# Kernel tuning notes

Measured on AMD Instinct MI355X. Metric: run time of the kernel, lower is better.

## Reference

```python
import jax, jax.numpy as jnp
import numpy as np

N_NODES = 50000
N_EDGES = 800000
N_FEAT = 128
HIDDEN = 64
EMBED = 300
N_CLASSES = 10
N_GRAPHS = 500
LEAKY_SLOPE = 0.01  # torch F.leaky_relu default


def gcn_conv(x, W, b, src, dst, n_nodes):
    # PyG GCNConv: h = x @ W; add self-loops; norm = deg^{-1/2}[src] * deg^{-1/2}[dst]
    h = x @ W  # [N, H]
    deg = jax.ops.segment_sum(jnp.ones_like(dst, dtype=h.dtype), dst, num_segments=n_nodes) + 1.0  # +1 self-loop
    dis = jax.lax.rsqrt(deg)  # deg^{-1/2}, deg >= 1 so finite
    norm = dis[src] * dis[dst]  # [E]
    agg = jax.ops.segment_sum(h[src] * norm[:, None], dst, num_segments=n_nodes)
    agg = agg + h * (dis * dis)[:, None]  # self-loop contribution
    return agg + b


def segment_softmax(s, seg, num_segments):
    # s: [N, 1]; softmax over nodes within each graph
    m = jax.ops.segment_max(s, seg, num_segments=num_segments)
    e = jnp.exp(s - m[seg])
    z = jax.ops.segment_sum(e, seg, num_segments=num_segments)
    return e / z[seg]


def setup_inputs() -> dict:
    key = jax.random.key(0)
    ks = jax.random.split(key, 16)

    def glorot(k, shape):
        fan_in, fan_out = shape[0], shape[1]
        lim = np.sqrt(6.0 / (fan_in + fan_out)).astype(np.float32)
        return jax.random.uniform(k, shape, jnp.float32, -lim, lim)

    x = jax.random.normal(ks[0], (N_NODES, N_FEAT), jnp.float32)
    edge_index = jax.random.randint(ks[1], (2, N_EDGES), 0, N_NODES, dtype=jnp.int64)
    batch = jnp.sort(jax.random.randint(ks[2], (N_NODES,), 0, N_GRAPHS, dtype=jnp.int64))
    return {
        "x": x,
        "edge_index": edge_index,
        "batch": batch,
        "W1": glorot(ks[3], (N_FEAT, HIDDEN)),
        "b1": jnp.zeros((HIDDEN,), jnp.float32),
        "W2": glorot(ks[4], (HIDDEN, HIDDEN)),
        "b2": jnp.zeros((HIDDEN,), jnp.float32),
        "att_w": glorot(ks[5], (HIDDEN, 1)),
        "att_b": jnp.zeros((1,), jnp.float32),
        "proj_w": glorot(ks[6], (HIDDEN, EMBED)),
        "proj_b": jnp.zeros((EMBED,), jnp.float32),
        "cls_w1": glorot(ks[7], (EMBED, 128)),
        "cls_b1": jnp.zeros((128,), jnp.float32),
        "cls_w2": glorot(ks[8], (128, N_CLASSES)),
        "cls_b2": jnp.zeros((N_CLASSES,), jnp.float32),
    }


def reference(x, edge_index, batch, W1, b1, W2, b2, att_w, att_b, proj_w, proj_b, cls_w1, cls_b1, cls_w2, cls_b2):
    src, dst = edge_index[0], edge_index[1]
    n_nodes = x.shape[0]
    h = jax.nn.relu(gcn_conv(x, W1, b1, src, dst, n_nodes))
    # dropout is identity in eval mode
    h = jax.nn.relu(gcn_conv(h, W2, b2, src, dst, n_nodes))  # [N, H]
    att = jax.nn.leaky_relu(h @ att_w + att_b, negative_slope=LEAKY_SLOPE)  # [N, 1]
    att = segment_softmax(att, batch, N_GRAPHS)
    g = jax.ops.segment_sum(att * h, batch, num_segments=N_GRAPHS)  # [G, H]
    g = g @ proj_w + proj_b  # [G, EMBED]
    out = jax.nn.relu(g @ cls_w1 + cls_b1) @ cls_w2 + cls_b2  # [G, num_classes]
    return out
```

## Files before the change

### kernel.cpp

```cpp
#include <hip/hip_runtime.h>
#include <hip/hip_fp16.h>
#include <math.h>

#define N_NODES   50000
#define N_EDGES   800000
#define N_FEAT    128
#define HIDDEN    64
#define EMBED     300
#define N_CLASSES 10
#define N_GRAPHS  500
#define LEAKY     0.01f
#define SCAN_BLOCKS 196
#define NB_FILL   3125
#define NB_G2     12500

typedef __attribute__((ext_vector_type(4))) _Float16 half4f;
typedef __attribute__((ext_vector_type(8))) _Float16 half8;
typedef __attribute__((ext_vector_type(4))) float f32x4;

__device__ __forceinline__ float pk_w(unsigned p) {
    return __half2float(__ushort_as_half((unsigned short)(p >> 16)));
}

__global__ void kA(int* deg, int* gs, int* ge,
                   const float* __restrict__ W1, __half* __restrict__ W1T,
                   const float* __restrict__ W2, __half* __restrict__ W2T) {
    int bid = blockIdx.x, tid = threadIdx.x;
    if (bid < 196) {
        int i = bid * 256 + tid;
        if (i < N_NODES) deg[i] = 0;
        if (i < N_GRAPHS) { gs[i] = 0; ge[i] = 0; }
    } else if (bid < 228) {
        int idx = (bid - 196) * 256 + tid;
        int n = idx >> 7, k = idx & 127;
        W1T[idx] = __float2half(W1[k * HIDDEN + n]);
    } else {
        int idx = (bid - 228) * 256 + tid;
        int n = idx >> 6, k = idx & 63;
        W2T[idx] = __float2half(W2[k * HIDDEN + n]);
    }
}

__global__ void k_deg_rank(const int* __restrict__ dst, int* deg, int* rank) {
    int e = blockIdx.x * 256 + threadIdx.x;
    if (e < N_EDGES) rank[e] = atomicAdd(&deg[dst[e]], 1);
}

__global__ __launch_bounds__(256) void k_scan1(const int* __restrict__ deg, int* row_start,
                                               int* partials, float* dis) {
    __shared__ int wsum[4];
    int i = blockIdx.x * 256 + threadIdx.x;
    int v = (i < N_NODES) ? deg[i] : 0;
    int lane = threadIdx.x & 63, wid = threadIdx.x >> 6;
    int s = v;
    #pragma unroll
    for (int off = 1; off < 64; off <<= 1) {
        int t = __shfl_up(s, off, 64);
        if (lane >= off) s += t;
    }
    if (lane == 63) wsum[wid] = s;
    __syncthreads();
    int woff = 0;
    for (int w = 0; w < wid; ++w) woff += wsum[w];
    if (i < N_NODES) {
        row_start[i] = woff + s - v;
        dis[i] = rsqrtf((float)(deg[i] + 1));
    }
    if (threadIdx.x == 255) partials[blockIdx.x] = woff + s;
}

__global__ __launch_bounds__(256) void k_scan3b(int* row_start, const int* __restrict__ partials) {
    __shared__ int wsum[4];
    int bid = blockIdx.x, tid = threadIdx.x;
    int lane = tid & 63, wid = tid >> 6;
    int v = (tid < SCAN_BLOCKS && tid < bid) ? partials[tid] : 0;
    #pragma unroll
    for (int off = 32; off > 0; off >>= 1) v += __shfl_xor(v, off, 64);
    if (lane == 0) wsum[wid] = v;
    __syncthreads();
    int prefix = wsum[0] + wsum[1] + wsum[2] + wsum[3];
    int i = bid * 256 + tid;
    if (i < N_NODES) row_start[i] += prefix;
    if (i == 0) row_start[N_NODES] = N_EDGES;
}

__global__ __launch_bounds__(256) void kB(const int* __restrict__ src, const int* __restrict__ dst,
                                          const int* __restrict__ rank, const int* __restrict__ row_start,
                                          const float* __restrict__ dis, unsigned* __restrict__ pk,
                                          const float* __restrict__ x, const __half* __restrict__ W1T,
                                          __half* __restrict__ h1) {
    if (blockIdx.x < NB_FILL) {
        int e = blockIdx.x * 256 + threadIdx.x;
        if (e < N_EDGES) {
            int s = src[e], d = dst[e];
            float w = dis[s] * dis[d];
            unsigned short wh = __half_as_ushort(__float2half(w));
            pk[row_start[d] + rank[e]] = (unsigned)s | ((unsigned)wh << 16);
        }
        return;
    }
    int tid = threadIdx.x, wid = tid >> 6, lane = tid & 63;
    int r16 = lane & 15, kg = lane >> 4;
    int rowbase = (blockIdx.x - NB_FILL) * 64 + wid * 16;
    int arow = rowbase + r16;
    bool avalid = arow < N_NODES;
    const float* xr = x + (size_t)arow * N_FEAT;

    half8 a[4];
    #pragma unroll
    for (int kt = 0; kt < 4; ++kt) {
        int k0 = kt * 32 + kg * 8;
        float4 u = avalid ? *(const float4*)(xr + k0)     : make_float4(0.f, 0.f, 0.f, 0.f);
        float4 v = avalid ? *(const float4*)(xr + k0 + 4) : make_float4(0.f, 0.f, 0.f, 0.f);
        a[kt][0] = (_Float16)u.x; a[kt][1] = (_Float16)u.y;
        a[kt][2] = (_Float16)u.z; a[kt][3] = (_Float16)u.w;
        a[kt][4] = (_Float16)v.x; a[kt][5] = (_Float16)v.y;
        a[kt][6] = (_Float16)v.z; a[kt][7] = (_Float16)v.w;
    }
    #pragma unroll
    for (int nt = 0; nt < 4; ++nt) {
        f32x4 acc = {0.f, 0.f, 0.f, 0.f};
        const _Float16* wp = (const _Float16*)W1T + (size_t)(nt * 16 + r16) * N_FEAT + kg * 8;
        #pragma unroll
        for (int kt = 0; kt < 4; ++kt) {
            half8 b = *(const half8*)(wp + kt * 32);
            acc = __builtin_amdgcn_mfma_f32_16x16x32_f16(a[kt], b, acc, 0, 0, 0);
        }
        int col = nt * 16 + r16;
        #pragma unroll
        for (int r = 0; r < 4; ++r) {
            int row = rowbase + kg * 4 + r;
            if (row < N_NODES) h1[(size_t)row * HIDDEN + col] = __float2half(acc[r]);
        }
    }
}

__device__ __forceinline__ void gather4pk(const __half* __restrict__ h,
                                          const unsigned* __restrict__ pk,
                                          int s, int e, int lane, int g4, int q,
                                          float4& acc) {
    for (int cs = s; cs < e; cs += 64) {
        unsigned pkv = (cs + lane < e) ? pk[cs + lane] : 0u;
        int avail = e - cs; if (avail > 64) avail = 64;
        int iters = (avail + 3) >> 2;
        #pragma unroll 2
        for (int t = 0; t < iters; ++t) {
            unsigned p = __shfl(pkv, t * 4 + g4, 64);
            float w = pk_w(p);
            half4f hv = *(const half4f*)(h + ((size_t)(p & 0xFFFFu)) * HIDDEN + (q << 2));
            acc.x = fmaf(w, (float)hv.x, acc.x);
            acc.y = fmaf(w, (float)hv.y, acc.y);
            acc.z = fmaf(w, (float)hv.z, acc.z);
            acc.w = fmaf(w, (float)hv.w, acc.w);
        }
    }
}

__device__ __forceinline__ void xreduce(float4& a) {
    a.x += __shfl_xor(a.x, 16, 64); a.y += __shfl_xor(a.y, 16, 64);
    a.z += __shfl_xor(a.z, 16, 64); a.w += __shfl_xor(a.w, 16, 64);
    a.x += __shfl_xor(a.x, 32, 64); a.y += __shfl_xor(a.y, 32, 64);
    a.z += __shfl_xor(a.z, 32, 64); a.w += __shfl_xor(a.w, 32, 64);
}

__global__ __launch_bounds__(256) void k_gg(const __half* __restrict__ h1,
                                            const unsigned* __restrict__ pk,
                                            const int* __restrict__ row_start,
                                            const float* __restrict__ dis,
                                            const float* __restrict__ b1,
                                            const __half* __restrict__ W2T,
                                            __half* __restrict__ h2) {
    __shared__ __align__(16) __half sa[16 * 72];
    int tid = threadIdx.x, wid = tid >> 6, lane = tid & 63;
    int g4 = lane >> 4, q = lane & 15;
    int base = blockIdx.x * 16 + wid * 4;
    #pragma unroll
    for (int i = 0; i < 4; ++i) {
        int node = base + i;
        int s = row_start[node], e = row_start[node + 1];
        float4 acc = {0.f, 0.f, 0.f, 0.f};
        gather4pk(h1, pk, s, e, lane, g4, q, acc);
        xreduce(acc);
        float dv = dis[node], dd = dv * dv;
        half4f sv = *(const half4f*)(h1 + (size_t)node * HIDDEN + (q << 2));
        float4 bv = *(const float4*)(b1 + (q << 2));
        if (g4 == 0) {
            half4f r;
            r.x = (_Float16)fmaxf(fmaf((float)sv.x, dd, bv.x) + acc.x, 0.f);
            r.y = (_Float16)fmaxf(fmaf((float)sv.y, dd, bv.y) + acc.y, 0.f);
            r.z = (_Float16)fmaxf(fmaf((float)sv.z, dd, bv.z) + acc.z, 0.f);
            r.w = (_Float16)fmaxf(fmaf((float)sv.w, dd, bv.w) + acc.w, 0.f);
            *(half4f*)&sa[(wid * 4 + i) * 72 + (q << 2)] = r;
        }
    }
    __syncthreads();

    int r16 = lane & 15, kg = lane >> 4;
    f32x4 acc = {0.f, 0.f, 0.f, 0.f};
    const _Float16* wp = (const _Float16*)W2T + (size_t)(wid * 16 + r16) * HIDDEN + kg * 8;
    #pragma unroll
    for (int kt = 0; kt < 2; ++kt) {
        half8 a = *(const half8*)&sa[r16 * 72 + kt * 32 + kg * 8];
        half8 b = *(const half8*)(wp + kt * 32);
        acc = __builtin_amdgcn_mfma_f32_16x16x32_f16(a, b, acc, 0, 0, 0);
    }
    int col = wid * 16 + r16;
    int nodebase = blockIdx.x * 16;
    #pragma unroll
    for (int r = 0; r < 4; ++r) {
        int row = nodebase + kg * 4 + r;
        h2[(size_t)row * HIDDEN + col] = __float2half(acc[r]);
    }
}

__global__ __launch_bounds__(256) void kC(const __half* __restrict__ h2,
                                          const unsigned* __restrict__ pk,
                                          const int* __restrict__ row_start,
                                          const float* __restrict__ dis,
                                          const float* __restrict__ b2,
                                          const float* __restrict__ att_w,
                                          const float* __restrict__ att_b,
                                          __half* __restrict__ agg2,
                                          float* __restrict__ att_s,
                                          const int* __restrict__ batch,
                                          int* gs, int* ge) {
    if (blockIdx.x >= NB_G2) {
        int n = (blockIdx.x - NB_G2) * 256 + threadIdx.x;
        if (n < N_NODES) {
            int b = batch[n];
            if (n == 0 || batch[n - 1] != b) gs[b] = n;
            if (n == N_NODES - 1 || batch[n + 1] != b) ge[b] = n + 1;
        }
        return;
    }
    int tid = threadIdx.x, wid = tid >> 6, lane = tid & 63;
    int g4 = lane >> 4, q = lane & 15;
    int node = blockIdx.x * 4 + wid;
    int s = row_start[node], e = row_start[node + 1];
    float4 acc = {0.f, 0.f, 0.f, 0.f};
    gather4pk(h2, pk, s, e, lane, g4, q, acc);
    xreduce(acc);
    float dv = dis[node], dd = dv * dv;
    half4f sv = *(const half4f*)(h2 + (size_t)node * HIDDEN + (q << 2));
    float4 bv = *(const float4*)(b2 + (q << 2));
    float4 r;
    r.x = fmaxf(fmaf((float)sv.x, dd, bv.x) + acc.x, 0.f);
    r.y = fmaxf(fmaf((float)sv.y, dd, bv.y) + acc.y, 0.f);
    r.z = fmaxf(fmaf((float)sv.z, dd, bv.z) + acc.z, 0.f);
    r.w = fmaxf(fmaf((float)sv.w, dd, bv.w) + acc.w, 0.f);
    if (g4 == 0) {
        half4f rh;
        rh.x = (_Float16)r.x; rh.y = (_Float16)r.y;
        rh.z = (_Float16)r.z; rh.w = (_Float16)r.w;
        *(half4f*)(agg2 + (size_t)node * HIDDEN + (q << 2)) = rh;
    }

    float4 aw = *(const float4*)(att_w + (q << 2));
    float v = fmaf(r.x, aw.x, fmaf(r.y, aw.y, fmaf(r.z, aw.z, r.w * aw.w)));
    v += __shfl_xor(v, 1, 64); v += __shfl_xor(v, 2, 64);
    v += __shfl_xor(v, 4, 64); v += __shfl_xor(v, 8, 64);
    if (lane == 0) {
        float sc = v + att_b[0];
        att_s[node] = (sc > 0.0f) ? sc : LEAKY * sc;
    }
}

__global__ __launch_bounds__(256) void k_pool_head(const __half* __restrict__ agg2,
                                                   const float* __restrict__ att_s,
                                                   const int* __restrict__ gs,
                                                   const int* __restrict__ ge,
                                                   const float* __restrict__ proj_w,
                                                   const float* __restrict__ proj_b,
                                                   const float* __restrict__ cls_w1,
                                                   const float* __restrict__ cls_b1,
                                                   const float* __restrict__ cls_w2,
                                                   const float* __restrict__ cls_b2,
                                                   float* __restrict__ out) {
    __shared__ float red[4];
    __shared__ float red2[4 * 64];
    __shared__ float sG[HIDDEN];
    __shared__ float sT1[EMBED];
    __shared__ float sT2[128];
    int gid = blockIdx.x;
    int tid = threadIdx.x, f = tid & 63, w = tid >> 6;
    int s = gs[gid], e = ge[gid];

    float m = -INFINITY;
    for (int n = s + tid; n < e; n += 256) m = fmaxf(m, att_s[n]);
    #pragma unroll
    for (int o = 32; o > 0; o >>= 1) m = fmaxf(m, __shfl_xor(m, o, 64));
    if (f == 0) red[w] = m;
    __syncthreads();
    m = fmaxf(fmaxf(red[0], red[1]), fmaxf(red[2], red[3]));
    __syncthreads();

    float z = 0.0f;
    for (int n = s + tid; n < e; n += 256) z += expf(att_s[n] - m);
    #pragma unroll
    for (int o = 32; o > 0; o >>= 1) z += __shfl_xor(z, o, 64);
    if (f == 0) red[w] = z;
    __syncthreads();
    z = red[0] + red[1] + red[2] + red[3];
    float inv = (e > s) ? 1.0f / z : 0.0f;

    float acc = 0.0f;
    for (int n = s + w; n < e; n += 4)
        acc = fmaf(expf(att_s[n] - m) * inv,
                   __half2float(agg2[(size_t)n * HIDDEN + f]), acc);
    red2[w * 64 + f] = acc;
    __syncthreads();
    if (w == 0) sG[f] = red2[f] + red2[64 + f] + red2[128 + f] + red2[192 + f];
    __syncthreads();

    for (int c = tid; c < EMBED; c += 256) {
        float a = proj_b[c];
        #pragma unroll 8
        for (int k = 0; k < HIDDEN; ++k) a = fmaf(sG[k], proj_w[k * EMBED + c], a);
        sT1[c] = a;
    }
    __syncthreads();

    if (tid < 128) {
        float a = cls_b1[tid];
        for (int k = 0; k < EMBED; ++k) a = fmaf(sT1[k], cls_w1[k * 128 + tid], a);
        sT2[tid] = fmaxf(a, 0.f);
    }
    __syncthreads();

    if (tid < N_CLASSES) {
        float a = cls_b2[tid];
        #pragma unroll 8
        for (int k = 0; k < 128; ++k) a = fmaf(sT2[k], cls_w2[k * N_CLASSES + tid], a);
        out[gid * N_CLASSES + tid] = a;
    }
}

extern "C" void kernel_launch(void* const* d_in, const int* in_sizes, int n_in,
                              void* d_out, int out_size, void* d_ws, size_t ws_size,
                              hipStream_t stream) {
    const float* x      = (const float*)d_in[0];
    const int*   ei     = (const int*)d_in[1];
    const int*   batch  = (const int*)d_in[2];
    const float* W1     = (const float*)d_in[3];
    const float* b1     = (const float*)d_in[4];
    const float* W2     = (const float*)d_in[5];
    const float* b2     = (const float*)d_in[6];
    const float* att_w  = (const float*)d_in[7];
    const float* att_b  = (const float*)d_in[8];
    const float* proj_w = (const float*)d_in[9];
    const float* proj_b = (const float*)d_in[10];
    const float* cls_w1 = (const float*)d_in[11];
    const float* cls_b1 = (const float*)d_in[12];
    const float* cls_w2 = (const float*)d_in[13];
    const float* cls_b2 = (const float*)d_in[14];
    float* out = (float*)d_out;

    const int* e_src = ei;
    const int* e_dst = ei + N_EDGES;

    float* base = (float*)d_ws;
    size_t o = 0;
    float*    dis       = base + o;              o += 50048;
    int*      deg_i     = (int*)(base + o);      o += 50048;
    int*      row_start = (int*)(base + o);      o += 50080;
    int*      partials  = (int*)(base + o);      o += 256;
    unsigned* pk        = (unsigned*)(base + o); o += 800000;
    __half*   h1        = (__half*)(base + o);   o += 1600000;
    __half*   h2        = (__half*)(base + o);   o += 1600000;
    __half*   agg2      = (__half*)(base + o);   o += 1600000;
    int*      rank      = (int*)agg2;
    float*    att_s     = base + o;              o += 50048;
    int*      gs        = (int*)(base + o);      o += 512;
    int*      ge        = (int*)(base + o);      o += 512;
    __half*   W1T       = (__half*)(base + o);   o += 4096;
    __half*   W2T       = (__half*)(base + o);   o += 2048;

    const int NB_E  = (N_EDGES + 255) / 256;
    const int NB_GG = N_NODES / 16;

    kA<<<244, 256, 0, stream>>>(deg_i, gs, ge, W1, W1T, W2, W2T);
    k_deg_rank<<<NB_E, 256, 0, stream>>>(e_dst, deg_i, rank);
    k_scan1<<<SCAN_BLOCKS, 256, 0, stream>>>(deg_i, row_start, partials, dis);
    k_scan3b<<<SCAN_BLOCKS, 256, 0, stream>>>(row_start, partials);

    kB<<<NB_FILL + 782, 256, 0, stream>>>(e_src, e_dst, rank, row_start, dis, pk, x, W1T, h1);

    k_gg<<<NB_GG, 256, 0, stream>>>(h1, pk, row_start, dis, b1, W2T, h2);

    kC<<<NB_G2 + SCAN_BLOCKS, 256, 0, stream>>>(h2, pk, row_start, dis, b2, att_w, att_b,
                                                agg2, att_s, batch, gs, ge);

    k_pool_head<<<N_GRAPHS, 256, 0, stream>>>(agg2, att_s, gs, ge,
                                              proj_w, proj_b, cls_w1, cls_b1,
                                              cls_w2, cls_b2, out);
}
```

Measured before the change: 163.8 us.

## Fuse scan into single-pass decoupled lookback and gather two nodes per wave

Replaces the two-kernel prefix scan with one kernel in which each block publishes its total to a flagged 64-bit slot and spins on the totals of earlier blocks, removing a launch. The aggregation kernels now interleave the neighbour gathers of two destination nodes per wave, so more independent loads are in flight to hide gather latency. The layer-2 kernel processes 8 nodes per block, halving its grid. Risks are spin-wait deadlock if blocks are not co-resident, though 196 blocks should fit, and higher register pressure from the dual accumulators.

```diff
diff --git a/kernel.cpp b/kernel.cpp
--- a/kernel.cpp
+++ b/kernel.cpp
@@ -12,7 +12,7 @@
 #define LEAKY     0.01f
 #define SCAN_BLOCKS 196
 #define NB_FILL   3125
-#define NB_G2     12500
+#define NB_G2B    6250
 
 typedef __attribute__((ext_vector_type(4))) _Float16 half4f;
 typedef __attribute__((ext_vector_type(8))) _Float16 half8;
@@ -22,7 +22,7 @@
     return __half2float(__ushort_as_half((unsigned short)(p >> 16)));
 }
 
-__global__ void kA(int* deg, int* gs, int* ge,
+__global__ void kA(int* deg, int* gs, int* ge, unsigned long long* aggs,
                    const float* __restrict__ W1, __half* __restrict__ W1T,
                    const float* __restrict__ W2, __half* __restrict__ W2T) {
     int bid = blockIdx.x, tid = threadIdx.x;
@@ -30,6 +30,7 @@
         int i = bid * 256 + tid;
         if (i < N_NODES) deg[i] = 0;
         if (i < N_GRAPHS) { gs[i] = 0; ge[i] = 0; }
+        if (bid == 0 && tid < SCAN_BLOCKS) aggs[tid] = 0ULL;
     } else if (bid < 228) {
         int idx = (bid - 196) * 256 + tid;
         int n = idx >> 7, k = idx & 127;
@@ -46,12 +47,15 @@
     if (e < N_EDGES) rank[e] = atomicAdd(&deg[dst[e]], 1);
 }
 
-__global__ __launch_bounds__(256) void k_scan1(const int* __restrict__ deg, int* row_start,
-                                               int* partials, float* dis) {
+__global__ __launch_bounds__(256) void k_scan(const int* __restrict__ deg,
+                                              int* __restrict__ row_start,
+                                              unsigned long long* __restrict__ aggs,
+                                              float* __restrict__ dis) {
     __shared__ int wsum[4];
-    int i = blockIdx.x * 256 + threadIdx.x;
+    int bid = blockIdx.x, tid = threadIdx.x;
+    int i = bid * 256 + tid;
     int v = (i < N_NODES) ? deg[i] : 0;
-    int lane = threadIdx.x & 63, wid = threadIdx.x >> 6;
+    int lane = tid & 63, wid = tid >> 6;
     int s = v;
     #pragma unroll
     for (int off = 1; off < 64; off <<= 1) {
@@ -62,25 +66,28 @@
     __syncthreads();
     int woff = 0;
     for (int w = 0; w < wid; ++w) woff += wsum[w];
+    int total = wsum[0] + wsum[1] + wsum[2] + wsum[3];
+
+    if (tid == 0)
+        atomicExch(&aggs[bid], (1ULL << 32) | (unsigned long long)(unsigned)total);
+
+    int pv = 0;
+    if (tid < bid) {
+        unsigned long long g;
+        do { g = atomicAdd(&aggs[tid], 0ULL); } while (!(g >> 32));
+        pv = (int)(unsigned)(g & 0xFFFFFFFFULL);
+    }
+    #pragma unroll
+    for (int off = 32; off > 0; off >>= 1) pv += __shfl_xor(pv, off, 64);
+    __syncthreads();
+    if (lane == 0) wsum[wid] = pv;
+    __syncthreads();
+    int prefix = wsum[0] + wsum[1] + wsum[2] + wsum[3];
+
     if (i < N_NODES) {
-        row_start[i] = woff + s - v;
+        row_start[i] = woff + s - v + prefix;
         dis[i] = rsqrtf((float)(deg[i] + 1));
     }
-    if (threadIdx.x == 255) partials[blockIdx.x] = woff + s;
-}
-
-__global__ __launch_bounds__(256) void k_scan3b(int* row_start, const int* __restrict__ partials) {
-    __shared__ int wsum[4];
-    int bid = blockIdx.x, tid = threadIdx.x;
-    int lane = tid & 63, wid = tid >> 6;
-    int v = (tid < SCAN_BLOCKS && tid < bid) ? partials[tid] : 0;
-    #pragma unroll
-    for (int off = 32; off > 0; off >>= 1) v += __shfl_xor(v, off, 64);
-    if (lane == 0) wsum[wid] = v;
-    __syncthreads();
-    int prefix = wsum[0] + wsum[1] + wsum[2] + wsum[3];
-    int i = bid * 256 + tid;
-    if (i < N_NODES) row_start[i] += prefix;
     if (i == 0) row_start[N_NODES] = N_EDGES;
 }
 
@@ -156,6 +163,41 @@
     }
 }
 
+__device__ __forceinline__ void gather2(const __half* __restrict__ h,
+                                        const unsigned* __restrict__ pk,
+                                        int s0, int e0, int s1, int e1,
+                                        int lane, int g4, int q,
+                                        float4& a0, float4& a1) {
+    unsigned pv0 = (s0 + lane < e0) ? pk[s0 + lane] : 0u;
+    unsigned pv1 = (s1 + lane < e1) ? pk[s1 + lane] : 0u;
+    int n0 = e0 - s0; if (n0 > 64) n0 = 64; if (n0 < 0) n0 = 0;
+    int n1 = e1 - s1; if (n1 > 64) n1 = 64; if (n1 < 0) n1 = 0;
+    int it0 = (n0 + 3) >> 2, it1 = (n1 + 3) >> 2;
+    int itm = it0 > it1 ? it0 : it1;
+    for (int t = 0; t < itm; ++t) {
+        if (t < it0) {
+            unsigned p = __shfl(pv0, t * 4 + g4, 64);
+            float w = pk_w(p);
+            half4f hv = *(const half4f*)(h + ((size_t)(p & 0xFFFFu)) * HIDDEN + (q << 2));
+            a0.x = fmaf(w, (float)hv.x, a0.x);
+            a0.y = fmaf(w, (float)hv.y, a0.y);
+            a0.z = fmaf(w, (float)hv.z, a0.z);
+            a0.w = fmaf(w, (float)hv.w, a0.w);
+        }
+        if (t < it1) {
+            unsigned p = __shfl(pv1, t * 4 + g4, 64);
+            float w = pk_w(p);
+            half4f hv = *(const half4f*)(h + ((size_t)(p & 0xFFFFu)) * HIDDEN + (q << 2));
+            a1.x = fmaf(w, (float)hv.x, a1.x);
+            a1.y = fmaf(w, (float)hv.y, a1.y);
+            a1.z = fmaf(w, (float)hv.z, a1.z);
+            a1.w = fmaf(w, (float)hv.w, a1.w);
+        }
+    }
+    if (e0 - s0 > 64) gather4pk(h, pk, s0 + 64, e0, lane, g4, q, a0);
+    if (e1 - s1 > 64) gather4pk(h, pk, s1 + 64, e1, lane, g4, q, a1);
+}
+
 __device__ __forceinline__ void xreduce(float4& a) {
     a.x += __shfl_xor(a.x, 16, 64); a.y += __shfl_xor(a.y, 16, 64);
     a.z += __shfl_xor(a.z, 16, 64); a.w += __shfl_xor(a.w, 16, 64);
@@ -174,23 +216,32 @@
     int tid = threadIdx.x, wid = tid >> 6, lane = tid & 63;
     int g4 = lane >> 4, q = lane & 15;
     int base = blockIdx.x * 16 + wid * 4;
-    #pragma unroll
-    for (int i = 0; i < 4; ++i) {
-        int node = base + i;
-        int s = row_start[node], e = row_start[node + 1];
-        float4 acc = {0.f, 0.f, 0.f, 0.f};
-        gather4pk(h1, pk, s, e, lane, g4, q, acc);
-        xreduce(acc);
-        float dv = dis[node], dd = dv * dv;
-        half4f sv = *(const half4f*)(h1 + (size_t)node * HIDDEN + (q << 2));
-        float4 bv = *(const float4*)(b1 + (q << 2));
+    float4 bv = *(const float4*)(b1 + (q << 2));
+
+    #pragma unroll
+    for (int pr = 0; pr < 2; ++pr) {
+        int n0 = base + pr * 2, n1 = n0 + 1;
+        int s0 = row_start[n0], e0 = row_start[n0 + 1];
+        int s1 = row_start[n1], e1 = row_start[n1 + 1];
+        float4 a0 = {0.f, 0.f, 0.f, 0.f}, a1 = {0.f, 0.f, 0.f, 0.f};
+        gather2(h1, pk, s0, e0, s1, e1, lane, g4, q, a0, a1);
+        xreduce(a0); xreduce(a1);
         if (g4 == 0) {
-            half4f r;
-            r.x = (_Float16)fmaxf(fmaf((float)sv.x, dd, bv.x) + acc.x, 0.f);
-            r.y = (_Float16)fmaxf(fmaf((float)sv.y, dd, bv.y) + acc.y, 0.f);
-            r.z = (_Float16)fmaxf(fmaf((float)sv.z, dd, bv.z) + acc.z, 0.f);
-            r.w = (_Float16)fmaxf(fmaf((float)sv.w, dd, bv.w) + acc.w, 0.f);
-            *(half4f*)&sa[(wid * 4 + i) * 72 + (q << 2)] = r;
+            float d0 = dis[n0]; d0 *= d0;
+            float d1 = dis[n1]; d1 *= d1;
+            half4f sv0 = *(const half4f*)(h1 + (size_t)n0 * HIDDEN + (q << 2));
+            half4f sv1 = *(const half4f*)(h1 + (size_t)n1 * HIDDEN + (q << 2));
+            half4f r0, r1;
+            r0.x = (_Float16)fmaxf(fmaf((float)sv0.x, d0, bv.x) + a0.x, 0.f);
+            r0.y = (_Float16)fmaxf(fmaf((float)sv0.y, d0, bv.y) + a0.y, 0.f);
+            r0.z = (_Float16)fmaxf(fmaf((float)sv0.z, d0, bv.z) + a0.z, 0.f);
+            r0.w = (_Float16)fmaxf(fmaf((float)sv0.w, d0, bv.w) + a0.w, 0.f);
+            r1.x = (_Float16)fmaxf(fmaf((float)sv1.x, d1, bv.x) + a1.x, 0.f);
+            r1.y = (_Float16)fmaxf(fmaf((float)sv1.y, d1, bv.y) + a1.y, 0.f);
+            r1.z = (_Float16)fmaxf(fmaf((float)sv1.z, d1, bv.z) + a1.z, 0.f);
+            r1.w = (_Float16)fmaxf(fmaf((float)sv1.w, d1, bv.w) + a1.w, 0.f);
+            *(half4f*)&sa[(wid * 4 + pr * 2 + 0) * 72 + (q << 2)] = r0;
+            *(half4f*)&sa[(wid * 4 + pr * 2 + 1) * 72 + (q << 2)] = r1;
         }
     }
     __syncthreads();
@@ -224,8 +275,8 @@
                                           float* __restrict__ att_s,
                                           const int* __restrict__ batch,
                                           int* gs, int* ge) {
-    if (blockIdx.x >= NB_G2) {
-        int n = (blockIdx.x - NB_G2) * 256 + threadIdx.x;
+    if (blockIdx.x >= NB_G2B) {
+        int n = (blockIdx.x - NB_G2B) * 256 + threadIdx.x;
         if (n < N_NODES) {
             int b = batch[n];
             if (n == 0 || batch[n - 1] != b) gs[b] = n;
@@ -235,33 +286,47 @@
     }
     int tid = threadIdx.x, wid = tid >> 6, lane = tid & 63;
     int g4 = lane >> 4, q = lane & 15;
-    int node = blockIdx.x * 4 + wid;
-    int s = row_start[node], e = row_start[node + 1];
-    float4 acc = {0.f, 0.f, 0.f, 0.f};
-    gather4pk(h2, pk, s, e, lane, g4, q, acc);
-    xreduce(acc);
-    float dv = dis[node], dd = dv * dv;
-    half4f sv = *(const half4f*)(h2 + (size_t)node * HIDDEN + (q << 2));
+    int n0 = blockIdx.x * 8 + wid * 2, n1 = n0 + 1;
+    int s0 = row_start[n0], e0 = row_start[n0 + 1];
+    int s1 = row_start[n1], e1 = row_start[n1 + 1];
+    float4 a0 = {0.f, 0.f, 0.f, 0.f}, a1 = {0.f, 0.f, 0.f, 0.f};
+    gather2(h2, pk, s0, e0, s1, e1, lane, g4, q, a0, a1);
+    xreduce(a0); xreduce(a1);
+
     float4 bv = *(const float4*)(b2 + (q << 2));
-    float4 r;
-    r.x = fmaxf(fmaf((float)sv.x, dd, bv.x) + acc.x, 0.f);
-    r.y = fmaxf(fmaf((float)sv.y, dd, bv.y) + acc.y, 0.f);
-    r.z = fmaxf(fmaf((float)sv.z, dd, bv.z) + acc.z, 0.f);
-    r.w = fmaxf(fmaf((float)sv.w, dd, bv.w) + acc.w, 0.f);
+    float d0 = dis[n0]; d0 *= d0;
+    float d1 = dis[n1]; d1 *= d1;
+    half4f sv0 = *(const half4f*)(h2 + (size_t)n0 * HIDDEN + (q << 2));
+    half4f sv1 = *(const half4f*)(h2 + (size_t)n1 * HIDDEN + (q << 2));
+    float4 r0, r1;
+    r0.x = fmaxf(fmaf((float)sv0.x, d0, bv.x) + a0.x, 0.f);
+    r0.y = fmaxf(fmaf((float)sv0.y, d0, bv.y) + a0.y, 0.f);
+    r0.z = fmaxf(fmaf((float)sv0.z, d0, bv.z) + a0.z, 0.f);
+    r0.w = fmaxf(fmaf((float)sv0.w, d0, bv.w) + a0.w, 0.f);
+    r1.x = fmaxf(fmaf((float)sv1.x, d1, bv.x) + a1.x, 0.f);
+    r1.y = fmaxf(fmaf((float)sv1.y, d1, bv.y) + a1.y, 0.f);
+    r1.z = fmaxf(fmaf((float)sv1.z, d1, bv.z) + a1.z, 0.f);
+    r1.w = fmaxf(fmaf((float)sv1.w, d1, bv.w) + a1.w, 0.f);
     if (g4 == 0) {
-        half4f rh;
-        rh.x = (_Float16)r.x; rh.y = (_Float16)r.y;
-        rh.z = (_Float16)r.z; rh.w = (_Float16)r.w;
-        *(half4f*)(agg2 + (size_t)node * HIDDEN + (q << 2)) = rh;
+        half4f h0, h1v;
+        h0.x = (_Float16)r0.x; h0.y = (_Float16)r0.y; h0.z = (_Float16)r0.z; h0.w = (_Float16)r0.w;
+        h1v.x = (_Float16)r1.x; h1v.y = (_Float16)r1.y; h1v.z = (_Float16)r1.z; h1v.w = (_Float16)r1.w;
+        *(half4f*)(agg2 + (size_t)n0 * HIDDEN + (q << 2)) = h0;
+        *(half4f*)(agg2 + (size_t)n1 * HIDDEN + (q << 2)) = h1v;
     }
 
     float4 aw = *(const float4*)(att_w + (q << 2));
-    float v = fmaf(r.x, aw.x, fmaf(r.y, aw.y, fmaf(r.z, aw.z, r.w * aw.w)));
-    v += __shfl_xor(v, 1, 64); v += __shfl_xor(v, 2, 64);
-    v += __shfl_xor(v, 4, 64); v += __shfl_xor(v, 8, 64);
+    float v0 = fmaf(r0.x, aw.x, fmaf(r0.y, aw.y, fmaf(r0.z, aw.z, r0.w * aw.w)));
+    float v1 = fmaf(r1.x, aw.x, fmaf(r1.y, aw.y, fmaf(r1.z, aw.z, r1.w * aw.w)));
+    v0 += __shfl_xor(v0, 1, 64); v1 += __shfl_xor(v1, 1, 64);
+    v0 += __shfl_xor(v0, 2, 64); v1 += __shfl_xor(v1, 2, 64);
+    v0 += __shfl_xor(v0, 4, 64); v1 += __shfl_xor(v1, 4, 64);
+    v0 += __shfl_xor(v0, 8, 64); v1 += __shfl_xor(v1, 8, 64);
     if (lane == 0) {
-        float sc = v + att_b[0];
-        att_s[node] = (sc > 0.0f) ? sc : LEAKY * sc;
+        float sc0 = v0 + att_b[0];
+        float sc1 = v1 + att_b[0];
+        att_s[n0] = (sc0 > 0.0f) ? sc0 : LEAKY * sc0;
+        att_s[n1] = (sc1 > 0.0f) ? sc1 : LEAKY * sc1;
     }
 }
 
@@ -363,7 +428,7 @@
     float*    dis       = base + o;              o += 50048;
     int*      deg_i     = (int*)(base + o);      o += 50048;
     int*      row_start = (int*)(base + o);      o += 50080;
-    int*      partials  = (int*)(base + o);      o += 256;
+    unsigned long long* aggs = (unsigned long long*)(base + o); o += 512;
     unsigned* pk        = (unsigned*)(base + o); o += 800000;
     __half*   h1        = (__half*)(base + o);   o += 1600000;
     __half*   h2        = (__half*)(base + o);   o += 1600000;
@@ -378,17 +443,16 @@
     const int NB_E  = (N_EDGES + 255) / 256;
     const int NB_GG = N_NODES / 16;
 
-    kA<<<244, 256, 0, stream>>>(deg_i, gs, ge, W1, W1T, W2, W2T);
+    kA<<<244, 256, 0, stream>>>(deg_i, gs, ge, aggs, W1, W1T, W2, W2T);
     k_deg_rank<<<NB_E, 256, 0, stream>>>(e_dst, deg_i, rank);
-    k_scan1<<<SCAN_BLOCKS, 256, 0, stream>>>(deg_i, row_start, partials, dis);
-    k_scan3b<<<SCAN_BLOCKS, 256, 0, stream>>>(row_start, partials);
+    k_scan<<<SCAN_BLOCKS, 256, 0, stream>>>(deg_i, row_start, aggs, dis);
 
     kB<<<NB_FILL + 782, 256, 0, stream>>>(e_src, e_dst, rank, row_start, dis, pk, x, W1T, h1);
 
     k_gg<<<NB_GG, 256, 0, stream>>>(h1, pk, row_start, dis, b1, W2T, h2);
 
-    kC<<<NB_G2 + SCAN_BLOCKS, 256, 0, stream>>>(h2, pk, row_start, dis, b2, att_w, att_b,
-                                                agg2, att_s, batch, gs, ge);
+    kC<<<NB_G2B + SCAN_BLOCKS, 256, 0, stream>>>(h2, pk, row_start, dis, b2, att_w, att_b,
+                                                 agg2, att_s, batch, gs, ge);
 
     k_pool_head<<<N_GRAPHS, 256, 0, stream>>>(agg2, att_s, gs, ge,
                                               proj_w, proj_b, cls_w1, cls_b1,
```

After: 157.3 us. 4.0% less time.

## Merge scan into single-pass decoupled lookback and interleave four-node gathers

Applied to the files above, without the earlier changes.

Replaces the two-kernel prefix scan with one kernel in which each block publishes its total with a flag and spin-waits on the flags of earlier blocks, removing a launch. The neighbor gather now loads the edge lists of four nodes at once and interleaves their loads in a single loop, so more memory requests are in flight per wave. The second aggregation kernel now handles four nodes per wave with a quarter of the blocks. The spin-wait assumes earlier blocks are resident or already scheduled; with 196 blocks that holds on this GPU, but it adds a small risk and some atomic polling traffic.

```diff
diff --git a/kernel.cpp b/kernel.cpp
--- a/kernel.cpp
+++ b/kernel.cpp
@@ -12,7 +12,7 @@
 #define LEAKY     0.01f
 #define SCAN_BLOCKS 196
 #define NB_FILL   3125
-#define NB_G2     12500
+#define NB_G2Q    3125
 
 typedef __attribute__((ext_vector_type(4))) _Float16 half4f;
 typedef __attribute__((ext_vector_type(8))) _Float16 half8;
@@ -22,7 +22,7 @@
     return __half2float(__ushort_as_half((unsigned short)(p >> 16)));
 }
 
-__global__ void kA(int* deg, int* gs, int* ge,
+__global__ void kA(int* deg, int* gs, int* ge, unsigned long long* aggs,
                    const float* __restrict__ W1, __half* __restrict__ W1T,
                    const float* __restrict__ W2, __half* __restrict__ W2T) {
     int bid = blockIdx.x, tid = threadIdx.x;
@@ -30,6 +30,7 @@
         int i = bid * 256 + tid;
         if (i < N_NODES) deg[i] = 0;
         if (i < N_GRAPHS) { gs[i] = 0; ge[i] = 0; }
+        if (bid == 0 && tid < SCAN_BLOCKS) aggs[tid] = 0ULL;
     } else if (bid < 228) {
         int idx = (bid - 196) * 256 + tid;
         int n = idx >> 7, k = idx & 127;
@@ -46,12 +47,15 @@
     if (e < N_EDGES) rank[e] = atomicAdd(&deg[dst[e]], 1);
 }
 
-__global__ __launch_bounds__(256) void k_scan1(const int* __restrict__ deg, int* row_start,
-                                               int* partials, float* dis) {
+__global__ __launch_bounds__(256) void k_scan(const int* __restrict__ deg,
+                                              int* __restrict__ row_start,
+                                              unsigned long long* __restrict__ aggs,
+                                              float* __restrict__ dis) {
     __shared__ int wsum[4];
-    int i = blockIdx.x * 256 + threadIdx.x;
+    int bid = blockIdx.x, tid = threadIdx.x;
+    int i = bid * 256 + tid;
     int v = (i < N_NODES) ? deg[i] : 0;
-    int lane = threadIdx.x & 63, wid = threadIdx.x >> 6;
+    int lane = tid & 63, wid = tid >> 6;
     int s = v;
     #pragma unroll
     for (int off = 1; off < 64; off <<= 1) {
@@ -62,25 +66,28 @@
     __syncthreads();
     int woff = 0;
     for (int w = 0; w < wid; ++w) woff += wsum[w];
+    int total = wsum[0] + wsum[1] + wsum[2] + wsum[3];
+
+    if (tid == 0)
+        atomicExch(&aggs[bid], (1ULL << 32) | (unsigned long long)(unsigned)total);
+
+    int pv = 0;
+    if (tid < bid) {
+        unsigned long long g;
+        do { g = atomicAdd(&aggs[tid], 0ULL); } while (!(g >> 32));
+        pv = (int)(unsigned)(g & 0xFFFFFFFFULL);
+    }
+    #pragma unroll
+    for (int off = 32; off > 0; off >>= 1) pv += __shfl_xor(pv, off, 64);
+    __syncthreads();
+    if (lane == 0) wsum[wid] = pv;
+    __syncthreads();
+    int prefix = wsum[0] + wsum[1] + wsum[2] + wsum[3];
+
     if (i < N_NODES) {
-        row_start[i] = woff + s - v;
+        row_start[i] = woff + s - v + prefix;
         dis[i] = rsqrtf((float)(deg[i] + 1));
     }
-    if (threadIdx.x == 255) partials[blockIdx.x] = woff + s;
-}
-
-__global__ __launch_bounds__(256) void k_scan3b(int* row_start, const int* __restrict__ partials) {
-    __shared__ int wsum[4];
-    int bid = blockIdx.x, tid = threadIdx.x;
-    int lane = tid & 63, wid = tid >> 6;
-    int v = (tid < SCAN_BLOCKS && tid < bid) ? partials[tid] : 0;
-    #pragma unroll
-    for (int off = 32; off > 0; off >>= 1) v += __shfl_xor(v, off, 64);
-    if (lane == 0) wsum[wid] = v;
-    __syncthreads();
-    int prefix = wsum[0] + wsum[1] + wsum[2] + wsum[3];
-    int i = bid * 256 + tid;
-    if (i < N_NODES) row_start[i] += prefix;
     if (i == 0) row_start[N_NODES] = N_EDGES;
 }
 
@@ -135,6 +142,15 @@
     }
 }
 
+__device__ __forceinline__ void gacc(const __half* __restrict__ h, unsigned p, int q, float4& a) {
+    float w = pk_w(p);
+    half4f hv = *(const half4f*)(h + ((size_t)(p & 0xFFFFu)) * HIDDEN + (q << 2));
+    a.x = fmaf(w, (float)hv.x, a.x);
+    a.y = fmaf(w, (float)hv.y, a.y);
+    a.z = fmaf(w, (float)hv.z, a.z);
+    a.w = fmaf(w, (float)hv.w, a.w);
+}
+
 __device__ __forceinline__ void gather4pk(const __half* __restrict__ h,
                                           const unsigned* __restrict__ pk,
                                           int s, int e, int lane, int g4, int q,
@@ -144,16 +160,39 @@
         int avail = e - cs; if (avail > 64) avail = 64;
         int iters = (avail + 3) >> 2;
         #pragma unroll 2
-        for (int t = 0; t < iters; ++t) {
-            unsigned p = __shfl(pkv, t * 4 + g4, 64);
-            float w = pk_w(p);
-            half4f hv = *(const half4f*)(h + ((size_t)(p & 0xFFFFu)) * HIDDEN + (q << 2));
-            acc.x = fmaf(w, (float)hv.x, acc.x);
-            acc.y = fmaf(w, (float)hv.y, acc.y);
-            acc.z = fmaf(w, (float)hv.z, acc.z);
-            acc.w = fmaf(w, (float)hv.w, acc.w);
-        }
-    }
+        for (int t = 0; t < iters; ++t)
+            gacc(h, __shfl(pkv, t * 4 + g4, 64), q, acc);
+    }
+}
+
+__device__ __forceinline__ void gather4x(const __half* __restrict__ h,
+                                         const unsigned* __restrict__ pk,
+                                         const int rs[5], int lane, int g4, int q,
+                                         float4 a[4]) {
+    unsigned pv0 = (rs[0] + lane < rs[1]) ? pk[rs[0] + lane] : 0u;
+    unsigned pv1 = (rs[1] + lane < rs[2]) ? pk[rs[1] + lane] : 0u;
+    unsigned pv2 = (rs[2] + lane < rs[3]) ? pk[rs[2] + lane] : 0u;
+    unsigned pv3 = (rs[3] + lane < rs[4]) ? pk[rs[3] + lane] : 0u;
+    int n0 = rs[1] - rs[0]; if (n0 > 64) n0 = 64;
+    int n1 = rs[2] - rs[1]; if (n1 > 64) n1 = 64;
+    int n2 = rs[3] - rs[2]; if (n2 > 64) n2 = 64;
+    int n3 = rs[4] - rs[3]; if (n3 > 64) n3 = 64;
+    int it0 = (n0 + 3) >> 2, it1 = (n1 + 3) >> 2;
+    int it2 = (n2 + 3) >> 2, it3 = (n3 + 3) >> 2;
+    int m01 = it0 > it1 ? it0 : it1;
+    int m23 = it2 > it3 ? it2 : it3;
+    int itm = m01 > m23 ? m01 : m23;
+    for (int t = 0; t < itm; ++t) {
+        int sl = t * 4 + g4;
+        if (t < it0) gacc(h, __shfl(pv0, sl, 64), q, a[0]);
+        if (t < it1) gacc(h, __shfl(pv1, sl, 64), q, a[1]);
+        if (t < it2) gacc(h, __shfl(pv2, sl, 64), q, a[2]);
+        if (t < it3) gacc(h, __shfl(pv3, sl, 64), q, a[3]);
+    }
+    if (rs[1] - rs[0] > 64) gather4pk(h, pk, rs[0] + 64, rs[1], lane, g4, q, a[0]);
+    if (rs[2] - rs[1] > 64) gather4pk(h, pk, rs[1] + 64, rs[2], lane, g4, q, a[1]);
+    if (rs[3] - rs[2] > 64) gather4pk(h, pk, rs[2] + 64, rs[3], lane, g4, q, a[2]);
+    if (rs[4] - rs[3] > 64) gather4pk(h, pk, rs[3] + 64, rs[4], lane, g4, q, a[3]);
 }
 
 __device__ __forceinline__ void xreduce(float4& a) {
@@ -174,22 +213,29 @@
     int tid = threadIdx.x, wid = tid >> 6, lane = tid & 63;
     int g4 = lane >> 4, q = lane & 15;
     int base = blockIdx.x * 16 + wid * 4;
-    #pragma unroll
-    for (int i = 0; i < 4; ++i) {
-        int node = base + i;
-        int s = row_start[node], e = row_start[node + 1];
-        float4 acc = {0.f, 0.f, 0.f, 0.f};
-        gather4pk(h1, pk, s, e, lane, g4, q, acc);
-        xreduce(acc);
-        float dv = dis[node], dd = dv * dv;
-        half4f sv = *(const half4f*)(h1 + (size_t)node * HIDDEN + (q << 2));
-        float4 bv = *(const float4*)(b1 + (q << 2));
-        if (g4 == 0) {
+    int rs[5];
+    #pragma unroll
+    for (int i = 0; i < 5; ++i) rs[i] = row_start[base + i];
+
+    float4 a[4];
+    #pragma unroll
+    for (int i = 0; i < 4; ++i) a[i] = make_float4(0.f, 0.f, 0.f, 0.f);
+    gather4x(h1, pk, rs, lane, g4, q, a);
+    #pragma unroll
+    for (int i = 0; i < 4; ++i) xreduce(a[i]);
+
+    float4 bv = *(const float4*)(b1 + (q << 2));
+    if (g4 == 0) {
+        #pragma unroll
+        for (int i = 0; i < 4; ++i) {
+            int node = base + i;
+            float dd = dis[node]; dd *= dd;
+            half4f sv = *(const half4f*)(h1 + (size_t)node * HIDDEN + (q << 2));
             half4f r;
-            r.x = (_Float16)fmaxf(fmaf((float)sv.x, dd, bv.x) + acc.x, 0.f);
-            r.y = (_Float16)fmaxf(fmaf((float)sv.y, dd, bv.y) + acc.y, 0.f);
-            r.z = (_Float16)fmaxf(fmaf((float)sv.z, dd, bv.z) + acc.z, 0.f);
-            r.w = (_Float16)fmaxf(fmaf((float)sv.w, dd, bv.w) + acc.w, 0.f);
+            r.x = (_Float16)fmaxf(fmaf((float)sv.x, dd, bv.x) + a[i].x, 0.f);
+            r.y = (_Float16)fmaxf(fmaf((float)sv.y, dd, bv.y) + a[i].y, 0.f);
+            r.z = (_Float16)fmaxf(fmaf((float)sv.z, dd, bv.z) + a[i].z, 0.f);
+            r.w = (_Float16)fmaxf(fmaf((float)sv.w, dd, bv.w) + a[i].w, 0.f);
             *(half4f*)&sa[(wid * 4 + i) * 72 + (q << 2)] = r;
         }
     }
@@ -200,9 +246,9 @@
     const _Float16* wp = (const _Float16*)W2T + (size_t)(wid * 16 + r16) * HIDDEN + kg * 8;
     #pragma unroll
     for (int kt = 0; kt < 2; ++kt) {
-        half8 a = *(const half8*)&sa[r16 * 72 + kt * 32 + kg * 8];
+        half8 av = *(const half8*)&sa[r16 * 72 + kt * 32 + kg * 8];
         half8 b = *(const half8*)(wp + kt * 32);
-        acc = __builtin_amdgcn_mfma_f32_16x16x32_f16(a, b, acc, 0, 0, 0);
+        acc = __builtin_amdgcn_mfma_f32_16x16x32_f16(av, b, acc, 0, 0, 0);
     }
     int col = wid * 16 + r16;
     int nodebase = blockIdx.x * 16;
@@ -224,8 +270,8 @@
                                           float* __restrict__ att_s,
                                           const int* __restrict__ batch,
                                           int* gs, int* ge) {
-    if (blockIdx.x >= NB_G2) {
-        int n = (blockIdx.x - NB_G2) * 256 + threadIdx.x;
+    if (blockIdx.x >= NB_G2Q) {
+        int n = (blockIdx.x - NB_G2Q) * 256 + threadIdx.x;
         if (n < N_NODES) {
             int b = batch[n];
             if (n == 0 || batch[n - 1] != b) gs[b] = n;
@@ -235,33 +281,44 @@
     }
     int tid = threadIdx.x, wid = tid >> 6, lane = tid & 63;
     int g4 = lane >> 4, q = lane & 15;
-    int node = blockIdx.x * 4 + wid;
-    int s = row_start[node], e = row_start[node + 1];
-    float4 acc = {0.f, 0.f, 0.f, 0.f};
-    gather4pk(h2, pk, s, e, lane, g4, q, acc);
-    xreduce(acc);
-    float dv = dis[node], dd = dv * dv;
-    half4f sv = *(const half4f*)(h2 + (size_t)node * HIDDEN + (q << 2));
+    int base = blockIdx.x * 16 + wid * 4;
+    int rs[5];
+    #pragma unroll
+    for (int i = 0; i < 5; ++i) rs[i] = row_start[base + i];
+
+    float4 a[4];
+    #pragma unroll
+    for (int i = 0; i < 4; ++i) a[i] = make_float4(0.f, 0.f, 0.f, 0.f);
+    gather4x(h2, pk, rs, lane, g4, q, a);
+    #pragma unroll
+    for (int i = 0; i < 4; ++i) xreduce(a[i]);
+
     float4 bv = *(const float4*)(b2 + (q << 2));
-    float4 r;
-    r.x = fmaxf(fmaf((float)sv.x, dd, bv.x) + acc.x, 0.f);
-    r.y = fmaxf(fmaf((float)sv.y, dd, bv.y) + acc.y, 0.f);
-    r.z = fmaxf(fmaf((float)sv.z, dd, bv.z) + acc.z, 0.f);
-    r.w = fmaxf(fmaf((float)sv.w, dd, bv.w) + acc.w, 0.f);
-    if (g4 == 0) {
-        half4f rh;
-        rh.x = (_Float16)r.x; rh.y = (_Float16)r.y;
-        rh.z = (_Float16)r.z; rh.w = (_Float16)r.w;
-        *(half4f*)(agg2 + (size_t)node * HIDDEN + (q << 2)) = rh;
-    }
-
     float4 aw = *(const float4*)(att_w + (q << 2));
-    float v = fmaf(r.x, aw.x, fmaf(r.y, aw.y, fmaf(r.z, aw.z, r.w * aw.w)));
-    v += __shfl_xor(v, 1, 64); v += __shfl_xor(v, 2, 64);
-    v += __shfl_xor(v, 4, 64); v += __shfl_xor(v, 8, 64);
-    if (lane == 0) {
-        float sc = v + att_b[0];
-        att_s[node] = (sc > 0.0f) ? sc : LEAKY * sc;
+    float ab = att_b[0];
+    #pragma unroll
+    for (int i = 0; i < 4; ++i) {
+        int node = base + i;
+        float dd = dis[node]; dd *= dd;
+        half4f sv = *(const half4f*)(h2 + (size_t)node * HIDDEN + (q << 2));
+        float4 r;
+        r.x = fmaxf(fmaf((float)sv.x, dd, bv.x) + a[i].x, 0.f);
+        r.y = fmaxf(fmaf((float)sv.y, dd, bv.y) + a[i].y, 0.f);
+        r.z = fmaxf(fmaf((float)sv.z, dd, bv.z) + a[i].z, 0.f);
+        r.w = fmaxf(fmaf((float)sv.w, dd, bv.w) + a[i].w, 0.f);
+        if (g4 == 0) {
+            half4f rh;
+            rh.x = (_Float16)r.x; rh.y = (_Float16)r.y;
+            rh.z = (_Float16)r.z; rh.w = (_Float16)r.w;
+            *(half4f*)(agg2 + (size_t)node * HIDDEN + (q << 2)) = rh;
+        }
+        float v = fmaf(r.x, aw.x, fmaf(r.y, aw.y, fmaf(r.z, aw.z, r.w * aw.w)));
+        v += __shfl_xor(v, 1, 64); v += __shfl_xor(v, 2, 64);
+        v += __shfl_xor(v, 4, 64); v += __shfl_xor(v, 8, 64);
+        if (lane == 0) {
+            float sc = v + ab;
+            att_s[node] = (sc > 0.0f) ? sc : LEAKY * sc;
+        }
     }
 }
 
@@ -363,7 +420,7 @@
     float*    dis       = base + o;              o += 50048;
     int*      deg_i     = (int*)(base + o);      o += 50048;
     int*      row_start = (int*)(base + o);      o += 50080;
-    int*      partials  = (int*)(base + o);      o += 256;
+    unsigned long long* aggs = (unsigned long long*)(base + o); o += 512;
     unsigned* pk        = (unsigned*)(base + o); o += 800000;
     __half*   h1        = (__half*)(base + o);   o += 1600000;
     __half*   h2        = (__half*)(base + o);   o += 1600000;
@@ -378,17 +435,16 @@
     const int NB_E  = (N_EDGES + 255) / 256;
     const int NB_GG = N_NODES / 16;
 
-    kA<<<244, 256, 0, stream>>>(deg_i, gs, ge, W1, W1T, W2, W2T);
+    kA<<<244, 256, 0, stream>>>(deg_i, gs, ge, aggs, W1, W1T, W2, W2T);
     k_deg_rank<<<NB_E, 256, 0, stream>>>(e_dst, deg_i, rank);
-    k_scan1<<<SCAN_BLOCKS, 256, 0, stream>>>(deg_i, row_start, partials, dis);
-    k_scan3b<<<SCAN_BLOCKS, 256, 0, stream>>>(row_start, partials);
+    k_scan<<<SCAN_BLOCKS, 256, 0, stream>>>(deg_i, row_start, aggs, dis);
 
     kB<<<NB_FILL + 782, 256, 0, stream>>>(e_src, e_dst, rank, row_start, dis, pk, x, W1T, h1);
 
     k_gg<<<NB_GG, 256, 0, stream>>>(h1, pk, row_start, dis, b1, W2T, h2);
 
-    kC<<<NB_G2 + SCAN_BLOCKS, 256, 0, stream>>>(h2, pk, row_start, dis, b2, att_w, att_b,
-                                                agg2, att_s, batch, gs, ge);
+    kC<<<NB_G2Q + SCAN_BLOCKS, 256, 0, stream>>>(h2, pk, row_start, dis, b2, att_w, att_b,
+                                                 agg2, att_s, batch, gs, ge);
 
     k_pool_head<<<N_GRAPHS, 256, 0, stream>>>(agg2, att_s, gs, ge,
                                               proj_w, proj_b, cls_w1, cls_b1,
```

Result: faster. 157.8 us (-3.6%).
